# Kernel tuning notes

Hardware: AMD Instinct MI355X
Metric: run time of the kernel (lower is better)

## Reference

```python
import jax, jax.numpy as jnp
import numpy as np

NUM_NODES = 4
D = 1024            # hidden dim and dims of s_0, s_1; initial_input_dims = [D, D, 2D]
NUM_OPS = 5         # candidate ops per MixedLayer: linear, relu, tanh, sigmoid, leaky_relu(0.2)
NUM_LAYERS = 18     # sum_{i<4} (i+3)
BATCH = 4096

_ACTS = [
    lambda h: h,
    jax.nn.relu,
    jnp.tanh,
    jax.nn.sigmoid,
    lambda h: jax.nn.leaky_relu(h, 0.2),
]

def setup_inputs() -> dict:
    key = jax.random.key(0)
    ks = jax.random.split(key, 7)
    s_0 = jax.random.normal(ks[0], (BATCH, D), jnp.float32)
    s_1 = jax.random.normal(ks[1], (BATCH, D), jnp.float32)
    genotype = jax.random.uniform(ks[2], (NUM_LAYERS, NUM_OPS), jnp.float32)
    genotype = genotype / genotype.sum(-1, keepdims=True)  # softmax-like arch weights
    scale = 1.0 / np.sqrt(D)
    # 14 layers take a D-dim input; 4 layers (the cat(s_0,s_1) edge of each node) take 2D
    Ws = jax.random.normal(ks[3], (14, NUM_OPS, D, D), jnp.float32) * scale
    Wb = jax.random.normal(ks[4], (4, NUM_OPS, 2 * D, D), jnp.float32) * (scale / np.sqrt(2.0))
    bs = jax.random.normal(ks[5], (NUM_LAYERS, NUM_OPS, D), jnp.float32) * 0.01
    return {"s_0": s_0, "s_1": s_1, "genotype": genotype, "Ws": Ws, "Wb": Wb, "bs": bs}

def _mixed(x, W, b, w):
    # x: [B, in], W: [K, in, D], b: [K, D], w: [K]
    h = jnp.einsum('bi,kio->kbo', x, W) + b[:, None, :]
    out = 0.0
    for k, act in enumerate(_ACTS):
        out = out + w[k] * act(h[k])
    return out

def reference(s_0, s_1, genotype, Ws, Wb, bs):
    states = [s_0, s_1, jnp.concatenate([s_0, s_1], axis=-1)]
    offset, si, bi = 0, 0, 0
    for i in range(NUM_NODES):
        s = 0.0
        for j, cur in enumerate(states):
            l = offset + j
            if j == 2:  # edge from cat(s_0, s_1): input dim 2D
                W = Wb[bi]; bi += 1
            else:
                W = Ws[si]; si += 1
            s = s + _mixed(cur, W, bs[l], genotype[l])
        offset += len(states)
        states.append(s)
    return states[-1]
```

## Files before the change

kernel.cpp:

```cpp
#include <hip/hip_runtime.h>
#include <hip/hip_bf16.h>
#include <cstdint>
#include <cstddef>

typedef __attribute__((ext_vector_type(8))) short bf16x8;
typedef __attribute__((ext_vector_type(4))) float f32x4;

#define DEV __device__ __forceinline__

DEV unsigned short f2bf(float f) {
  unsigned int u = __float_as_uint(f);
  return (unsigned short)((u + 0x7fffu + ((u >> 16) & 1u)) >> 16);
}

DEV void gl_lds16(const unsigned short* g, unsigned short* l) {
  __builtin_amdgcn_global_load_lds(
      (__attribute__((address_space(1))) const void*)g,
      (__attribute__((address_space(3))) void*)l, 16, 0, 0);
}

__global__ __launch_bounds__(256) void cvt_kernel(const float* __restrict__ src,
                                                  unsigned short* __restrict__ dst) {
  size_t i = (size_t)blockIdx.x * 256 + threadIdx.x;
  float4 v = ((const float4*)src)[i];
  ushort4 o;
  o.x = f2bf(v.x); o.y = f2bf(v.y); o.z = f2bf(v.z); o.w = f2bf(v.w);
  ((ushort4*)dst)[i] = o;
}

__global__ __launch_bounds__(256) void transpose_kernel(const float* __restrict__ src,
                                                        unsigned short* __restrict__ dst,
                                                        int K) {
  __shared__ float tile[64][68];
  const int t = threadIdx.x;
  const int tpm = (K >> 6) * 16;
  const int mat = blockIdx.x / tpm;
  const int r = blockIdx.x % tpm;
  const int tk = r >> 4;
  const int tn = r & 15;
  const size_t sbase = (size_t)mat * K * 1024 + (size_t)tk * 64 * 1024 + (size_t)tn * 64;
#pragma unroll
  for (int p = 0; p < 4; ++p) {
    int row = p * 16 + (t >> 4);
    int c4 = (t & 15) * 4;
    float4 v = *(const float4*)&src[sbase + (size_t)row * 1024 + c4];
    *(float4*)&tile[row][c4] = v;
  }
  __syncthreads();
  const size_t dbase = (size_t)mat * 1024 * K + (size_t)tn * 64 * K + (size_t)tk * 64;
#pragma unroll
  for (int p = 0; p < 4; ++p) {
    int n = p * 16 + (t >> 4);
    int k4 = (t & 15) * 4;
    ushort4 o;
    o.x = f2bf(tile[k4 + 0][n]);
    o.y = f2bf(tile[k4 + 1][n]);
    o.z = f2bf(tile[k4 + 2][n]);
    o.w = f2bf(tile[k4 + 3][n]);
    *(ushort4*)&dst[dbase + (size_t)n * K + k4] = o;
  }
}

struct EdgeCfg {
  const unsigned short* xlo;
  const unsigned short* xhi;
  const unsigned short* wt;
  int inlen;
  int l;
};
struct NodeArgs {
  EdgeCfg e[6];
  int nedges;
};

template <int FINAL>
__global__ __launch_bounds__(256) void node_kernel(NodeArgs na,
                                                   const float* __restrict__ genotype,
                                                   const float* __restrict__ bs,
                                                   unsigned short* __restrict__ outb,
                                                   float* __restrict__ outf) {
  __shared__ unsigned short As[64 * 32];
  __shared__ unsigned short Bs[128 * 32];

  const int t = threadIdx.x;
  const int lane = t & 63;
  const int w = t >> 6;
  const int wm = (w & 1) * 32;
  const int wn = (w >> 1) * 64;
  const int bm = blockIdx.y * 64;
  const int bn = blockIdx.x * 128;
  const int l15 = lane & 15;
  const int l16 = lane >> 4;

  const int arow = t >> 2;
  const int acol = (t & 3) * 8;

  f32x4 sacc[2][4];
#pragma unroll
  for (int mi = 0; mi < 2; ++mi)
#pragma unroll
    for (int ni = 0; ni < 4; ++ni) sacc[mi][ni] = (f32x4){0.f, 0.f, 0.f, 0.f};

  for (int e = 0; e < na.nedges; ++e) {
    const int inlen = na.e[e].inlen;
    const unsigned short* xlo = na.e[e].xlo;
    const unsigned short* xhi = na.e[e].xhi;
    const unsigned short* wt0 = na.e[e].wt;
    const int l = na.e[e].l;
    const int nk = inlen >> 5;
    for (int k5 = 0; k5 < 5; ++k5) {
      const unsigned short* wtk = wt0 + (size_t)k5 * inlen * 1024;
      f32x4 hacc[2][4];
#pragma unroll
      for (int mi = 0; mi < 2; ++mi)
#pragma unroll
        for (int ni = 0; ni < 4; ++ni) hacc[mi][ni] = (f32x4){0.f, 0.f, 0.f, 0.f};

      for (int kt = 0; kt < nk; ++kt) {
        const int k0 = kt << 5;
        __syncthreads();
        const unsigned short* ax = (k0 < 1024) ? xlo : xhi;
        const int ak = k0 & 1023;
        gl_lds16(ax + (size_t)(bm + arow) * 1024 + ak + acol, As + t * 8);
        const unsigned short* wrow = wtk + (size_t)(bn + arow) * inlen + k0 + acol;
        gl_lds16(wrow, Bs + t * 8);
        gl_lds16(wrow + (size_t)64 * inlen, Bs + 2048 + t * 8);
        __syncthreads();

        bf16x8 af[2], bfr[4];
#pragma unroll
        for (int mi = 0; mi < 2; ++mi)
          af[mi] = *(const bf16x8*)&As[(wm + mi * 16 + l15) * 32 + l16 * 8];
#pragma unroll
        for (int ni = 0; ni < 4; ++ni)
          bfr[ni] = *(const bf16x8*)&Bs[(wn + ni * 16 + l15) * 32 + l16 * 8];
#pragma unroll
        for (int mi = 0; mi < 2; ++mi)
#pragma unroll
          for (int ni = 0; ni < 4; ++ni)
            hacc[mi][ni] = __builtin_amdgcn_mfma_f32_16x16x32_bf16(af[mi], bfr[ni],
                                                                   hacc[mi][ni], 0, 0, 0);
      }

      const float wlk = genotype[l * 5 + k5];
      const float* bv = bs + ((size_t)l * 5 + k5) * 1024;
#pragma unroll
      for (int ni = 0; ni < 4; ++ni) {
        const float bias = bv[bn + wn + ni * 16 + l15];
#pragma unroll
        for (int mi = 0; mi < 2; ++mi)
#pragma unroll
          for (int i = 0; i < 4; ++i) {
            float h = hacc[mi][ni][i] + bias;
            float a;
            if (k5 == 0) a = h;
            else if (k5 == 1) a = fmaxf(h, 0.f);
            else if (k5 == 2) a = 1.f - 2.f / (__expf(2.f * h) + 1.f);
            else if (k5 == 3) a = 1.f / (1.f + __expf(-h));
            else a = (h > 0.f) ? h : 0.2f * h;
            sacc[mi][ni][i] += wlk * a;
          }
      }
    }
  }

#pragma unroll
  for (int mi = 0; mi < 2; ++mi)
#pragma unroll
    for (int ni = 0; ni < 4; ++ni)
#pragma unroll
      for (int i = 0; i < 4; ++i) {
        const int row = bm + wm + mi * 16 + l16 * 4 + i;
        const int col = bn + wn + ni * 16 + l15;
        if (FINAL)
          outf[(size_t)row * 1024 + col] = sacc[mi][ni][i];
        else
          outb[(size_t)row * 1024 + col] = f2bf(sacc[mi][ni][i]);
      }
}

extern "C" void kernel_launch(void* const* d_in, const int* in_sizes, int n_in,
                              void* d_out, int out_size, void* d_ws, size_t ws_size,
                              hipStream_t stream) {
  const float* s0 = (const float*)d_in[0];
  const float* s1 = (const float*)d_in[1];
  const float* geno = (const float*)d_in[2];
  const float* Ws = (const float*)d_in[3];
  const float* Wb = (const float*)d_in[4];
  const float* bs = (const float*)d_in[5];

  unsigned short* WsT = (unsigned short*)d_ws;
  unsigned short* WbT = WsT + 70ull * 1024 * 1024;
  unsigned short* S0 = WbT + 20ull * 2048 * 1024;
  unsigned short* S1 = S0 + 4096ull * 1024;
  unsigned short* T0 = S1 + 4096ull * 1024;
  unsigned short* T1 = T0 + 4096ull * 1024;
  unsigned short* T2 = T1 + 4096ull * 1024;

  cvt_kernel<<<4096, 256, 0, stream>>>(s0, S0);
  cvt_kernel<<<4096, 256, 0, stream>>>(s1, S1);
  transpose_kernel<<<70 * 256, 256, 0, stream>>>(Ws, WsT, 1024);
  transpose_kernel<<<20 * 512, 256, 0, stream>>>(Wb, WbT, 2048);

  auto SE = [&](const unsigned short* x, int si, int l) {
    EdgeCfg c;
    c.xlo = x; c.xhi = x;
    c.wt = WsT + (size_t)si * 5 * 1024 * 1024;
    c.inlen = 1024; c.l = l;
    return c;
  };
  auto BE = [&](int bi, int l) {
    EdgeCfg c;
    c.xlo = S0; c.xhi = S1;
    c.wt = WbT + (size_t)bi * 5 * 2048 * 1024;
    c.inlen = 2048; c.l = l;
    return c;
  };

  dim3 grid(8, 64);
  {
    NodeArgs a{}; a.nedges = 3;
    a.e[0] = SE(S0, 0, 0); a.e[1] = SE(S1, 1, 1); a.e[2] = BE(0, 2);
    node_kernel<0><<<grid, 256, 0, stream>>>(a, geno, bs, T0, nullptr);
  }
  {
    NodeArgs a{}; a.nedges = 4;
    a.e[0] = SE(S0, 2, 3); a.e[1] = SE(S1, 3, 4); a.e[2] = BE(1, 5); a.e[3] = SE(T0, 4, 6);
    node_kernel<0><<<grid, 256, 0, stream>>>(a, geno, bs, T1, nullptr);
  }
  {
    NodeArgs a{}; a.nedges = 5;
    a.e[0] = SE(S0, 5, 7); a.e[1] = SE(S1, 6, 8); a.e[2] = BE(2, 9);
    a.e[3] = SE(T0, 7, 10); a.e[4] = SE(T1, 8, 11);
    node_kernel<0><<<grid, 256, 0, stream>>>(a, geno, bs, T2, nullptr);
  }
  {
    NodeArgs a{}; a.nedges = 6;
    a.e[0] = SE(S0, 9, 12); a.e[1] = SE(S1, 10, 13); a.e[2] = BE(3, 14);
    a.e[3] = SE(T0, 11, 15); a.e[4] = SE(T1, 12, 16); a.e[5] = SE(T2, 13, 17);
    node_kernel<1><<<grid, 256, 0, stream>>>(a, geno, bs, nullptr, (float*)d_out);
  }
}
```

Before: 3.009 ms.

## Split mixed ops across grid z and reduce node sums via float atomics

Each of the five candidate ops now runs in its own block along grid z, and block tiles grow from 64x128 to 128x128 for more reuse per LDS load. Partial node sums are combined with float atomic adds into an fp32 buffer, which a separate kernel then converts to bf16 and zeroes for the next node. This trades per-block serial work and accumulator reuse for more blocks and better tile reuse. The cost is extra atomic traffic, zero and convert kernels, and an order-dependent summation.

```diff
diff --git a/kernel.cpp b/kernel.cpp
--- a/kernel.cpp
+++ b/kernel.cpp
@@ -26,6 +26,21 @@
   ushort4 o;
   o.x = f2bf(v.x); o.y = f2bf(v.y); o.z = f2bf(v.z); o.w = f2bf(v.w);
   ((ushort4*)dst)[i] = o;
+}
+
+__global__ __launch_bounds__(256) void zero_kernel(float* __restrict__ p) {
+  size_t i = (size_t)blockIdx.x * 256 + threadIdx.x;
+  ((float4*)p)[i] = make_float4(0.f, 0.f, 0.f, 0.f);
+}
+
+__global__ __launch_bounds__(256) void cvtzero_kernel(float* __restrict__ s,
+                                                      unsigned short* __restrict__ dst) {
+  size_t i = (size_t)blockIdx.x * 256 + threadIdx.x;
+  float4 v = ((float4*)s)[i];
+  ushort4 o;
+  o.x = f2bf(v.x); o.y = f2bf(v.y); o.z = f2bf(v.z); o.w = f2bf(v.w);
+  ((ushort4*)dst)[i] = o;
+  ((float4*)s)[i] = make_float4(0.f, 0.f, 0.f, 0.f);
 }
 
 __global__ __launch_bounds__(256) void transpose_kernel(const float* __restrict__ src,
@@ -73,31 +88,30 @@
   int nedges;
 };
 
-template <int FINAL>
-__global__ __launch_bounds__(256) void node_kernel(NodeArgs na,
-                                                   const float* __restrict__ genotype,
-                                                   const float* __restrict__ bs,
-                                                   unsigned short* __restrict__ outb,
-                                                   float* __restrict__ outf) {
-  __shared__ unsigned short As[64 * 32];
+__global__ __launch_bounds__(256) void node_gemm(NodeArgs na,
+                                                 const float* __restrict__ genotype,
+                                                 const float* __restrict__ bs,
+                                                 float* __restrict__ sout) {
+  __shared__ unsigned short As[128 * 32];
   __shared__ unsigned short Bs[128 * 32];
 
   const int t = threadIdx.x;
   const int lane = t & 63;
   const int w = t >> 6;
-  const int wm = (w & 1) * 32;
+  const int wm = (w & 1) * 64;
   const int wn = (w >> 1) * 64;
-  const int bm = blockIdx.y * 64;
   const int bn = blockIdx.x * 128;
+  const int bm = blockIdx.y * 128;
+  const int kop = blockIdx.z;
   const int l15 = lane & 15;
   const int l16 = lane >> 4;
 
-  const int arow = t >> 2;
-  const int acol = (t & 3) * 8;
-
-  f32x4 sacc[2][4];
-#pragma unroll
-  for (int mi = 0; mi < 2; ++mi)
+  const int srow = t >> 2;
+  const int scol = (t & 3) * 8;
+
+  f32x4 sacc[4][4];
+#pragma unroll
+  for (int mi = 0; mi < 4; ++mi)
 #pragma unroll
     for (int ni = 0; ni < 4; ++ni) sacc[mi][ni] = (f32x4){0.f, 0.f, 0.f, 0.f};
 
@@ -105,77 +119,73 @@
     const int inlen = na.e[e].inlen;
     const unsigned short* xlo = na.e[e].xlo;
     const unsigned short* xhi = na.e[e].xhi;
-    const unsigned short* wt0 = na.e[e].wt;
+    const unsigned short* wtk = na.e[e].wt + (size_t)kop * inlen * 1024;
     const int l = na.e[e].l;
     const int nk = inlen >> 5;
-    for (int k5 = 0; k5 < 5; ++k5) {
-      const unsigned short* wtk = wt0 + (size_t)k5 * inlen * 1024;
-      f32x4 hacc[2][4];
-#pragma unroll
-      for (int mi = 0; mi < 2; ++mi)
-#pragma unroll
-        for (int ni = 0; ni < 4; ++ni) hacc[mi][ni] = (f32x4){0.f, 0.f, 0.f, 0.f};
-
-      for (int kt = 0; kt < nk; ++kt) {
-        const int k0 = kt << 5;
-        __syncthreads();
-        const unsigned short* ax = (k0 < 1024) ? xlo : xhi;
-        const int ak = k0 & 1023;
-        gl_lds16(ax + (size_t)(bm + arow) * 1024 + ak + acol, As + t * 8);
-        const unsigned short* wrow = wtk + (size_t)(bn + arow) * inlen + k0 + acol;
-        gl_lds16(wrow, Bs + t * 8);
-        gl_lds16(wrow + (size_t)64 * inlen, Bs + 2048 + t * 8);
-        __syncthreads();
-
-        bf16x8 af[2], bfr[4];
-#pragma unroll
-        for (int mi = 0; mi < 2; ++mi)
-          af[mi] = *(const bf16x8*)&As[(wm + mi * 16 + l15) * 32 + l16 * 8];
+
+    f32x4 hacc[4][4];
+#pragma unroll
+    for (int mi = 0; mi < 4; ++mi)
+#pragma unroll
+      for (int ni = 0; ni < 4; ++ni) hacc[mi][ni] = (f32x4){0.f, 0.f, 0.f, 0.f};
+
+    for (int kt = 0; kt < nk; ++kt) {
+      const int k0 = kt << 5;
+      __syncthreads();
+      const unsigned short* ax = (k0 < 1024) ? xlo : xhi;
+      const int ak = k0 & 1023;
+      gl_lds16(ax + (size_t)(bm + srow) * 1024 + ak + scol, As + t * 8);
+      gl_lds16(ax + (size_t)(bm + 64 + srow) * 1024 + ak + scol, As + 2048 + t * 8);
+      const unsigned short* wr = wtk + (size_t)(bn + srow) * inlen + k0 + scol;
+      gl_lds16(wr, Bs + t * 8);
+      gl_lds16(wr + (size_t)64 * inlen, Bs + 2048 + t * 8);
+      __syncthreads();
+
+      bf16x8 af[4], bfr[4];
+#pragma unroll
+      for (int mi = 0; mi < 4; ++mi)
+        af[mi] = *(const bf16x8*)&As[(wm + mi * 16 + l15) * 32 + l16 * 8];
+#pragma unroll
+      for (int ni = 0; ni < 4; ++ni)
+        bfr[ni] = *(const bf16x8*)&Bs[(wn + ni * 16 + l15) * 32 + l16 * 8];
+#pragma unroll
+      for (int mi = 0; mi < 4; ++mi)
 #pragma unroll
         for (int ni = 0; ni < 4; ++ni)
-          bfr[ni] = *(const bf16x8*)&Bs[(wn + ni * 16 + l15) * 32 + l16 * 8];
-#pragma unroll
-        for (int mi = 0; mi < 2; ++mi)
-#pragma unroll
-          for (int ni = 0; ni < 4; ++ni)
-            hacc[mi][ni] = __builtin_amdgcn_mfma_f32_16x16x32_bf16(af[mi], bfr[ni],
-                                                                   hacc[mi][ni], 0, 0, 0);
-      }
-
-      const float wlk = genotype[l * 5 + k5];
-      const float* bv = bs + ((size_t)l * 5 + k5) * 1024;
-#pragma unroll
-      for (int ni = 0; ni < 4; ++ni) {
-        const float bias = bv[bn + wn + ni * 16 + l15];
-#pragma unroll
-        for (int mi = 0; mi < 2; ++mi)
-#pragma unroll
-          for (int i = 0; i < 4; ++i) {
-            float h = hacc[mi][ni][i] + bias;
-            float a;
-            if (k5 == 0) a = h;
-            else if (k5 == 1) a = fmaxf(h, 0.f);
-            else if (k5 == 2) a = 1.f - 2.f / (__expf(2.f * h) + 1.f);
-            else if (k5 == 3) a = 1.f / (1.f + __expf(-h));
-            else a = (h > 0.f) ? h : 0.2f * h;
-            sacc[mi][ni][i] += wlk * a;
-          }
-      }
+          hacc[mi][ni] = __builtin_amdgcn_mfma_f32_16x16x32_bf16(af[mi], bfr[ni],
+                                                                 hacc[mi][ni], 0, 0, 0);
     }
-  }
-
-#pragma unroll
-  for (int mi = 0; mi < 2; ++mi)
+
+    const float wlk = genotype[l * 5 + kop];
+    const float* bv = bs + ((size_t)l * 5 + kop) * 1024;
+#pragma unroll
+    for (int ni = 0; ni < 4; ++ni) {
+      const float bias = bv[bn + wn + ni * 16 + l15];
+#pragma unroll
+      for (int mi = 0; mi < 4; ++mi)
+#pragma unroll
+        for (int i = 0; i < 4; ++i) {
+          float h = hacc[mi][ni][i] + bias;
+          float a;
+          if (kop == 0) a = h;
+          else if (kop == 1) a = fmaxf(h, 0.f);
+          else if (kop == 2) a = 1.f - 2.f / (__expf(2.f * h) + 1.f);
+          else if (kop == 3) a = 1.f / (1.f + __expf(-h));
+          else a = (h > 0.f) ? h : 0.2f * h;
+          sacc[mi][ni][i] += wlk * a;
+        }
+    }
+  }
+
+#pragma unroll
+  for (int mi = 0; mi < 4; ++mi)
 #pragma unroll
     for (int ni = 0; ni < 4; ++ni)
 #pragma unroll
       for (int i = 0; i < 4; ++i) {
         const int row = bm + wm + mi * 16 + l16 * 4 + i;
         const int col = bn + wn + ni * 16 + l15;
-        if (FINAL)
-          outf[(size_t)row * 1024 + col] = sacc[mi][ni][i];
-        else
-          outb[(size_t)row * 1024 + col] = f2bf(sacc[mi][ni][i]);
+        unsafeAtomicAdd(&sout[(size_t)row * 1024 + col], sacc[mi][ni][i]);
       }
 }
 
@@ -196,9 +206,12 @@
   unsigned short* T0 = S1 + 4096ull * 1024;
   unsigned short* T1 = T0 + 4096ull * 1024;
   unsigned short* T2 = T1 + 4096ull * 1024;
+  float* S = (float*)(T2 + 4096ull * 1024);
 
   cvt_kernel<<<4096, 256, 0, stream>>>(s0, S0);
   cvt_kernel<<<4096, 256, 0, stream>>>(s1, S1);
+  zero_kernel<<<4096, 256, 0, stream>>>(S);
+  zero_kernel<<<4096, 256, 0, stream>>>((float*)d_out);
   transpose_kernel<<<70 * 256, 256, 0, stream>>>(Ws, WsT, 1024);
   transpose_kernel<<<20 * 512, 256, 0, stream>>>(Wb, WbT, 2048);
 
@@ -217,27 +230,30 @@
     return c;
   };
 
-  dim3 grid(8, 64);
+  dim3 grid(8, 32, 5);
   {
     NodeArgs a{}; a.nedges = 3;
     a.e[0] = SE(S0, 0, 0); a.e[1] = SE(S1, 1, 1); a.e[2] = BE(0, 2);
-    node_kernel<0><<<grid, 256, 0, stream>>>(a, geno, bs, T0, nullptr);
+    node_gemm<<<grid, 256, 0, stream>>>(a, geno, bs, S);
+    cvtzero_kernel<<<4096, 256, 0, stream>>>(S, T0);
   }
   {
     NodeArgs a{}; a.nedges = 4;
     a.e[0] = SE(S0, 2, 3); a.e[1] = SE(S1, 3, 4); a.e[2] = BE(1, 5); a.e[3] = SE(T0, 4, 6);
-    node_kernel<0><<<grid, 256, 0, stream>>>(a, geno, bs, T1, nullptr);
+    node_gemm<<<grid, 256, 0, stream>>>(a, geno, bs, S);
+    cvtzero_kernel<<<4096, 256, 0, stream>>>(S, T1);
   }
   {
     NodeArgs a{}; a.nedges = 5;
     a.e[0] = SE(S0, 5, 7); a.e[1] = SE(S1, 6, 8); a.e[2] = BE(2, 9);
     a.e[3] = SE(T0, 7, 10); a.e[4] = SE(T1, 8, 11);
-    node_kernel<0><<<grid, 256, 0, stream>>>(a, geno, bs, T2, nullptr);
+    node_gemm<<<grid, 256, 0, stream>>>(a, geno, bs, S);
+    cvtzero_kernel<<<4096, 256, 0, stream>>>(S, T2);
   }
   {
     NodeArgs a{}; a.nedges = 6;
     a.e[0] = SE(S0, 9, 12); a.e[1] = SE(S1, 10, 13); a.e[2] = BE(3, 14);
     a.e[3] = SE(T0, 11, 15); a.e[4] = SE(T1, 12, 16); a.e[5] = SE(T2, 13, 17);
-    node_kernel<1><<<grid, 256, 0, stream>>>(a, geno, bs, nullptr, (float*)d_out);
-  }
-}
+    node_gemm<<<grid, 256, 0, stream>>>(a, geno, bs, (float*)d_out);
+  }
+}
```

Measured after the change: 2.851 ms. -5.3%, faster.
